# Performance work log

Hardware: AMD Instinct MI355X
Metric: run time of the kernel (lower is better)

Reference implementation:

```python
import jax, jax.numpy as jnp
import numpy as np

B = 4096
STATE_DIM = 64
OBS_DIM = 32
BASE_DEGREE = 8
TIME_STEPS = 96
EPS = 1e-7


def _degree(t):
    # get_degree: degree_params initialized to linspace(0,1,time_steps); used via .item() (static)
    p = float(t) / (TIME_STEPS - 1)
    scaled = 0.5 * (1.0 + np.sin(2.0 * np.pi * p))
    return BASE_DEGREE + int(2.0 * scaled)


def _cheby_fwd_and_jac(x, coeffs, degree):
    """ChebyKAN forward y[b,o] = sum_{i,d} coeffs[i,o,d] * cos(d*acos(clip(tanh(x[b,i]))))
    plus its analytic per-sample Jacobian J[b,o,i] (replaces the torch autograd loop)."""
    t_raw = jnp.tanh(x)                                   # [B, D]
    t_val = jnp.clip(t_raw, -1.0 + EPS, 1.0 - EPS)
    theta = jnp.arccos(t_val)                             # [B, D]
    dvals = jnp.arange(degree + 1, dtype=x.dtype)         # [deg+1]
    ang = theta[..., None] * dvals                        # [B, D, deg+1]
    cheb = jnp.cos(ang)
    ac = coeffs[..., : degree + 1]                        # [D, D, deg+1]
    y = jnp.einsum('bid,iod->bo', cheb, ac)               # [B, D]
    # d cheb / d x = d*sin(d*theta) * (1 - tanh(x)^2) * mask / sqrt(1 - t_val^2)
    mask = ((t_raw > -1.0 + EPS) & (t_raw < 1.0 - EPS)).astype(x.dtype)
    dtheta_dx = -(1.0 - t_raw * t_raw) * mask / jnp.sqrt(1.0 - t_val * t_val)  # [B, D]
    dcheb_dx = -dvals * jnp.sin(ang) * dtheta_dx[..., None]                    # [B, D, deg+1]
    jac = jnp.einsum('bid,iod->boi', dcheb_dx, ac)        # [B, D, D] = dY_o/dx_i
    return y, jac


def setup_inputs() -> dict:
    key = jax.random.key(0)
    ks = jax.random.split(key, 5)
    obs = jax.random.normal(ks[0], (B, OBS_DIM), jnp.float32)
    prev_state = jax.random.normal(ks[1], (B, STATE_DIM), jnp.float32)
    A = jax.random.normal(ks[2], (B, STATE_DIM, STATE_DIM), jnp.float32)
    prev_cov = A @ A.transpose(0, 2, 1) / STATE_DIM + jnp.eye(STATE_DIM, dtype=jnp.float32)  # SPD
    bound = 1.0 / np.sqrt(STATE_DIM * (BASE_DEGREE + 3))  # kaiming-uniform style
    coeffs = jax.random.uniform(ks[3], (STATE_DIM, STATE_DIM, BASE_DEGREE + 3), jnp.float32, -bound, bound)
    M = jax.random.normal(ks[4], (STATE_DIM, OBS_DIM), jnp.float32)
    q, _ = jnp.linalg.qr(M)                               # orthonormal columns
    obs_matrix = q.T.astype(jnp.float32)                  # [OBS_DIM, STATE_DIM], orthogonal rows
    log_Q_diag = jnp.zeros((STATE_DIM,), jnp.float32)
    log_R_diag = jnp.zeros((OBS_DIM,), jnp.float32)
    return dict(obs=obs, prev_state=prev_state, prev_cov=prev_cov, coeffs=coeffs,
                obs_matrix=obs_matrix, log_Q_diag=log_Q_diag, log_R_diag=log_R_diag, t=10)


def reference(obs, prev_state, prev_cov, coeffs, obs_matrix, log_Q_diag, log_R_diag, t):
    degree = _degree(t)
    state_pred, Fj = _cheby_fwd_and_jac(prev_state, coeffs, degree)   # [B,D], [B,D,D]
    q = jnp.exp(log_Q_diag)                                           # [D]
    r = jnp.exp(log_R_diag)                                           # [O]
    H = obs_matrix                                                    # [O, D]
    # cov_pred = F P F^T + Q
    cov_pred = jnp.einsum('bij,bjk,blk->bil', Fj, prev_cov, Fj) + jnp.diag(q)[None]
    obs_pred = state_pred @ H.T                                       # [B, O]
    residual = obs - obs_pred                                         # [B, O]
    # S = H Pp H^T + R
    S = jnp.einsum('ij,bjk,lk->bil', H, cov_pred, H) + jnp.diag(r)[None]
    S_inv = jnp.linalg.pinv(S)                                        # [B, O, O]
    PHt = jnp.einsum('bij,oj->bio', cov_pred, H)                      # [B, D, O]
    K = jnp.einsum('bio,bop->bip', PHt, S_inv)                        # [B, D, O]
    state_update = state_pred + jnp.einsum('bio,bo->bi', K, residual)
    I_KH = jnp.eye(STATE_DIM, dtype=cov_pred.dtype)[None] - jnp.einsum('bio,oj->bij', K, H)
    # Joseph form: (I-KH) Pp (I-KH)^T + K R K^T
    cov_update = (jnp.einsum('bij,bjk,blk->bil', I_KH, cov_pred, I_KH)
                  + jnp.einsum('bio,o,bjo->bij', K, r, K))
    cov_diag = jnp.diagonal(cov_update, axis1=1, axis2=2)
    return state_update, cov_update, cov_diag
```

## Files before the change

kernel.cpp:

```cpp
#include <hip/hip_runtime.h>
#include <math.h>


typedef float f4 __attribute__((ext_vector_type(4)));
typedef float f32x4 __attribute__((ext_vector_type(4)));
typedef short b16x8 __attribute__((ext_vector_type(8)));
typedef short b16x4 __attribute__((ext_vector_type(4)));
typedef unsigned int u32;
typedef unsigned int u32x4 __attribute__((ext_vector_type(4)));
typedef unsigned short u16;

#define EPSC 1e-7f
#define MFMA(a, b, c) __builtin_amdgcn_mfma_f32_16x16x32_bf16(a, b, c, 0, 0, 0)
static constexpr size_t CU_OFF = 4096 * 64;
static constexpr size_t CD_OFF = CU_OFF + 4096ull * 4096;

__device__ __forceinline__ void split2(float x, short &h, short &l) {
  u32 u = __float_as_uint(x);
  h = (short)(u >> 16);
  float rem = x - __uint_as_float(u & 0xffff0000u);
  l = (short)(__float_as_uint(rem) >> 16);
}
__device__ __forceinline__ u32 packsplit(float x) {
  u32 u = __float_as_uint(x) & 0xffff0000u;
  float rem = x - __uint_as_float(u);
  return u | (__float_as_uint(rem) >> 16);
}
__device__ __forceinline__ float unpackf(u32 v) {
  return __uint_as_float(v & 0xffff0000u) + __uint_as_float(v << 16);
}
union U8 { u32x4 u; b16x8 s; };
__device__ __forceinline__ void unpack8(u32x4 q0, u32x4 q1, b16x8 &hi,
                                        b16x8 &lo) {
  U8 H, L;
  H.u[0] = __builtin_amdgcn_perm(q0[1], q0[0], 0x07060302u);
  H.u[1] = __builtin_amdgcn_perm(q0[3], q0[2], 0x07060302u);
  H.u[2] = __builtin_amdgcn_perm(q1[1], q1[0], 0x07060302u);
  H.u[3] = __builtin_amdgcn_perm(q1[3], q1[2], 0x07060302u);
  L.u[0] = __builtin_amdgcn_perm(q0[1], q0[0], 0x05040100u);
  L.u[1] = __builtin_amdgcn_perm(q0[3], q0[2], 0x05040100u);
  L.u[2] = __builtin_amdgcn_perm(q1[1], q1[0], 0x05040100u);
  L.u[3] = __builtin_amdgcn_perm(q1[3], q1[2], 0x05040100u);
  hi = H.s;
  lo = L.s;
}
__device__ __forceinline__ void split8v(f4 a, f4 b, b16x8 &hi, b16x8 &lo) {
#pragma unroll
  for (int j = 0; j < 4; ++j) {
    short hh, ll;
    split2(a[j], hh, ll); hi[j] = hh; lo[j] = ll;
    split2(b[j], hh, ll); hi[4 + j] = hh; lo[4 + j] = ll;
  }
}

__global__ __launch_bounds__(256, 4) void kalman_fused(
    const float *__restrict__ obs, const float *__restrict__ prev_state,
    const float *__restrict__ prev_cov, const float *__restrict__ coeffs,
    const float *__restrict__ Hm, const float *__restrict__ logQ,
    const float *__restrict__ logR, const int *__restrict__ tptr,
    float *__restrict__ out) {
  __shared__ __align__(16) unsigned char pool[32768];
  u16 *sPh = (u16 *)(pool);
  u16 *sPl = (u16 *)(pool + 8192);
  u32 *sT = (u32 *)(pool);
  u32 *sPHt = (u32 *)(pool);
  u32 *sSpk = (u32 *)(pool + 8192);
  u32 *sK = (u32 *)(pool + 8192);
  u16 *sFh = (u16 *)(pool + 16384);
  u16 *sFl = (u16 *)(pool + 24576);
  u32 *sCov = (u32 *)(pool + 16384);
  float *sChT = (float *)(pool);
  float *sDcT = (float *)(pool + 3072);
  float *ypart = (float *)(pool + 6144);

  const int tid = (int)threadIdx.x;
  const int b = (int)blockIdx.x;
  const int w = tid >> 6;
  const int l = tid & 63;
  const int lr = l & 15;
  const int h = l >> 4;
  const int rowbase = (w == 0) ? 48 : 16 * (w - 1);

  f4 pr[4];
  {
    const float *Pg = prev_cov + (size_t)b * 4096;
#pragma unroll
    for (int e = 0; e < 4; ++e)
      pr[e] = *(const f4 *)(Pg + (rowbase + 4 * e + h) * 64 + lr * 4);
    if (tid < 64) {
      const int tval = tptr[0];
      const float ang = 6.28318530717958647f * ((float)tval / 95.0f);
      const int D = 9 + (int)(1.0f + sinf(ang));
      const float xx = prev_state[b * 64 + tid];
      const float tr_ = tanhf(xx);
      const float tv = fminf(fmaxf(tr_, -1.0f + EPSC), 1.0f - EPSC);
      const float sn = sqrtf(fmaxf(1.0f - tv * tv, 0.0f));
      const float mask = (tr_ > -1.0f + EPSC && tr_ < 1.0f - EPSC) ? 1.0f : 0.0f;
      const float dth = -(1.0f - tr_ * tr_) * mask / sn;
      float *ct = sChT + tid * 12;
      float *dt = sDcT + tid * 12;
      ct[0] = 1.f; ct[1] = tv; ct[11] = 0.f;
      dt[0] = 0.f; dt[1] = -dth * sn; dt[11] = 0.f;
      float cm2 = 1.f, cm1 = tv, sm2 = 0.f, sm1 = sn;
      const float tv2 = 2.f * tv;
#pragma unroll
      for (int d = 2; d <= 10; ++d) {
        const float cc = fmaf(tv2, cm1, -cm2);
        const float ss = fmaf(tv2, sm1, -sm2);
        ct[d] = (d < D) ? cc : 0.f;
        dt[d] = (d < D) ? (-dth * (float)d * ss) : 0.f;
        cm2 = cm1; cm1 = cc; sm2 = sm1; sm1 = ss;
      }
    }
  }
  __syncthreads();

  {
    const int o = tid & 63, g = tid >> 6;
    float yacc = 0.f;
    float fr[16];
#pragma unroll
    for (int ii = 0; ii < 16; ++ii) {
      const int i = g * 16 + ii;
      const float *cp = coeffs + (size_t)(i * 64 + o) * 11;
      f4 q0 = *(const f4 *)(cp);
      f4 q1 = *(const f4 *)(cp + 4);
      f4 q2 = *(const f4 *)(cp + 7);
      const float *ct = sChT + i * 12;
      const float *dt = sDcT + i * 12;
      f4 c0 = *(const f4 *)(ct), c1 = *(const f4 *)(ct + 4),
         c2 = *(const f4 *)(ct + 8);
      f4 e0 = *(const f4 *)(dt), e1 = *(const f4 *)(dt + 4),
         e2 = *(const f4 *)(dt + 8);
      float yac = q0[0];
      yac = fmaf(q0[1], c0[1], yac);
      yac = fmaf(q0[2], c0[2], yac);
      yac = fmaf(q0[3], c0[3], yac);
      yac = fmaf(q1[0], c1[0], yac);
      yac = fmaf(q1[1], c1[1], yac);
      yac = fmaf(q1[2], c1[2], yac);
      yac = fmaf(q1[3], c1[3], yac);
      yac = fmaf(q2[1], c2[0], yac);
      yac = fmaf(q2[2], c2[1], yac);
      yac = fmaf(q2[3], c2[2], yac);
      float fra = q0[1] * e0[1];
      fra = fmaf(q0[2], e0[2], fra);
      fra = fmaf(q0[3], e0[3], fra);
      fra = fmaf(q1[0], e1[0], fra);
      fra = fmaf(q1[1], e1[1], fra);
      fra = fmaf(q1[2], e1[2], fra);
      fra = fmaf(q1[3], e1[3], fra);
      fra = fmaf(q2[1], e2[0], fra);
      fra = fmaf(q2[2], e2[1], fra);
      fra = fmaf(q2[3], e2[2], fra);
      yacc += yac;
      fr[ii] = fra;
    }
    b16x8 fh0, fh1, fl0, fl1;
#pragma unroll
    for (int j = 0; j < 8; ++j) {
      short hh, ll;
      split2(fr[j], hh, ll); fh0[j] = hh; fl0[j] = ll;
      split2(fr[8 + j], hh, ll); fh1[j] = hh; fl1[j] = ll;
    }
    const int x = (o & 7) << 3;
    *(b16x8 *)(sFh + o * 64 + ((g * 16) ^ x)) = fh0;
    *(b16x8 *)(sFh + o * 64 + ((g * 16 + 8) ^ x)) = fh1;
    *(b16x8 *)(sFl + o * 64 + ((g * 16) ^ x)) = fl0;
    *(b16x8 *)(sFl + o * 64 + ((g * 16 + 8) ^ x)) = fl1;
    ypart[g * 64 + o] = yacc;
  }
  __syncthreads();

  float syl = 0.f, residreg = 0.f;
  if (w == 0)
    syl = ypart[l] + ypart[64 + l] + ypart[128 + l] + ypart[192 + l];
#pragma unroll
  for (int e = 0; e < 4; ++e) {
    const int row = rowbase + 4 * e + h;
    const int x = (row & 7) << 3;
    b16x4 h4, l4;
#pragma unroll
    for (int j = 0; j < 4; ++j) {
      short hh, ll;
      split2(pr[e][j], hh, ll);
      h4[j] = hh; l4[j] = ll;
    }
    *(b16x4 *)(sPh + row * 64 + ((lr * 4) ^ x)) = h4;
    *(b16x4 *)(sPl + row * 64 + ((lr * 4) ^ x)) = l4;
  }
  if (w == 0) {
    const int r = l & 31;
    float racc = obs[b * 32 + r];
    const float *Hr = Hm + r * 64;
#pragma unroll
    for (int c = 0; c < 64; c += 4) {
      f4 hv = *(const f4 *)(Hr + c);
#pragma unroll
      for (int j = 0; j < 4; ++j)
        racc = fmaf(-hv[j], __shfl(syl, c + j, 64), racc);
    }
    residreg = racc;
  }
  __syncthreads();

  f32x4 accT[4] = {{0.f, 0.f, 0.f, 0.f}, {0.f, 0.f, 0.f, 0.f},
                   {0.f, 0.f, 0.f, 0.f}, {0.f, 0.f, 0.f, 0.f}};
  {
    const int m = 16 * w + lr;
    const int xA = (m & 7) << 3;
#pragma unroll
    for (int kc = 0; kc < 2; ++kc) {
      const int k = kc * 32 + h * 8;
      b16x8 Ah = *(const b16x8 *)(sFh + m * 64 + (k ^ xA));
      b16x8 Al = *(const b16x8 *)(sFl + m * 64 + (k ^ xA));
#pragma unroll
      for (int t = 0; t < 4; ++t) {
        const int n = t * 16 + lr;
        const int xB = (n & 7) << 3;
        b16x8 Bh = *(const b16x8 *)(sPh + n * 64 + (k ^ xB));
        b16x8 Bl = *(const b16x8 *)(sPl + n * 64 + (k ^ xB));
        accT[t] = MFMA(Ah, Bh, accT[t]);
        accT[t] = MFMA(Al, Bh, accT[t]);
        accT[t] = MFMA(Ah, Bl, accT[t]);
      }
    }
  }
  __syncthreads();
  {
    const int r0 = 16 * w + h * 4;
#pragma unroll
    for (int t = 0; t < 4; ++t)
#pragma unroll
      for (int j = 0; j < 4; ++j) {
        const int rr = r0 + j, cc = t * 16 + lr;
        sT[rr * 64 + (cc ^ ((rr & 7) << 2))] = packsplit(accT[t][j]);
      }
  }

  f32x4 accC[4] = {{0.f, 0.f, 0.f, 0.f}, {0.f, 0.f, 0.f, 0.f},
                   {0.f, 0.f, 0.f, 0.f}, {0.f, 0.f, 0.f, 0.f}};
  {
    const int m = 16 * w + lr;
    const int xA = (m & 7) << 2;
    const u32 *Tb = sT + m * 64;
#pragma unroll
    for (int kc = 0; kc < 2; ++kc) {
      const int k = kc * 32 + h * 8;
      u32x4 q0 = *(const u32x4 *)(Tb + (k ^ xA));
      u32x4 q1 = *(const u32x4 *)(Tb + ((k + 4) ^ xA));
      b16x8 Ah, Al;
      unpack8(q0, q1, Ah, Al);
#pragma unroll
      for (int t = 0; t < 4; ++t) {
        const int n = t * 16 + lr;
        const int xB = (n & 7) << 3;
        b16x8 Bh = *(const b16x8 *)(sFh + n * 64 + (k ^ xB));
        b16x8 Bl = *(const b16x8 *)(sFl + n * 64 + (k ^ xB));
        accC[t] = MFMA(Ah, Bh, accC[t]);
        accC[t] = MFMA(Al, Bh, accC[t]);
        accC[t] = MFMA(Ah, Bl, accC[t]);
      }
    }
  }
  __syncthreads();
  {
    const int r0 = 16 * w + h * 4;
    f4 lq = *(const f4 *)(logQ + r0);
    float qv[4];
#pragma unroll
    for (int j = 0; j < 4; ++j) qv[j] = expf(lq[j]);
#pragma unroll
    for (int t = 0; t < 4; ++t)
#pragma unroll
      for (int j = 0; j < 4; ++j) {
        const int rr = r0 + j, cc = t * 16 + lr;
        float v = accC[t][j];
        if (rr == cc) v += qv[j];
        sCov[rr * 64 + (cc ^ ((rr & 7) << 2))] = packsplit(v);
      }
  }

  {
    f32x4 acc[2] = {{0.f, 0.f, 0.f, 0.f}, {0.f, 0.f, 0.f, 0.f}};
    const int m = 16 * w + lr;
    const int xA = (m & 7) << 2;
    const u32 *Cb = sCov + m * 64;
#pragma unroll
    for (int kc = 0; kc < 2; ++kc) {
      const int k = kc * 32 + h * 8;
      u32x4 q0 = *(const u32x4 *)(Cb + (k ^ xA));
      u32x4 q1 = *(const u32x4 *)(Cb + ((k + 4) ^ xA));
      b16x8 Ah, Al;
      unpack8(q0, q1, Ah, Al);
#pragma unroll
      for (int t = 0; t < 2; ++t) {
        const int n = t * 16 + lr;
        const float *Hr = Hm + n * 64 + k;
        f4 b0 = *(const f4 *)(Hr);
        f4 b1 = *(const f4 *)(Hr + 4);
        b16x8 Bh, Bl;
        split8v(b0, b1, Bh, Bl);
        acc[t] = MFMA(Ah, Bh, acc[t]);
        acc[t] = MFMA(Al, Bh, acc[t]);
        acc[t] = MFMA(Ah, Bl, acc[t]);
      }
    }
    const int r0 = 16 * w + h * 4;
#pragma unroll
    for (int t = 0; t < 2; ++t)
#pragma unroll
      for (int j = 0; j < 4; ++j) {
        const int rr = r0 + j, cc = t * 16 + lr;
        sPHt[rr * 32 + (cc ^ ((rr & 7) << 2))] = packsplit(acc[t][j]);
      }
  }
  __syncthreads();

  {
    const int tr = w >> 1, tc = w & 1;
    f32x4 acc = {0.f, 0.f, 0.f, 0.f};
    const int m = tr * 16 + lr;
    const int n = tc * 16 + lr;
#pragma unroll
    for (int kc = 0; kc < 2; ++kc) {
      const int k = kc * 32 + h * 8;
      const float *Hr = Hm + m * 64 + k;
      f4 a0 = *(const f4 *)(Hr);
      f4 a1 = *(const f4 *)(Hr + 4);
      b16x8 Ah, Al;
      split8v(a0, a1, Ah, Al);
      u32x4 q0, q1;
#pragma unroll
      for (int j = 0; j < 4; ++j)
        q0[j] = sPHt[(k + j) * 32 + (n ^ (j << 2))];
#pragma unroll
      for (int j = 0; j < 4; ++j)
        q1[j] = sPHt[(k + 4 + j) * 32 + (n ^ ((4 + j) << 2))];
      b16x8 Bh, Bl;
      unpack8(q0, q1, Bh, Bl);
      acc = MFMA(Ah, Bh, acc);
      acc = MFMA(Al, Bh, acc);
      acc = MFMA(Ah, Bl, acc);
    }
    const int r0s = tr * 16 + h * 4;
    f4 lrv = *(const f4 *)(logR + r0s);
#pragma unroll
    for (int j = 0; j < 4; ++j) {
      const int rr = r0s + j, cc = tc * 16 + lr;
      float v = acc[j];
      if (rr == cc) v += expf(lrv[j]);
      sSpk[rr * 32 + (cc ^ ((rr & 7) << 2))] = packsplit(v);
    }
  }
  __syncthreads();

  if (w == 0) {
    const int mr = l >> 1, half = l & 1;
    const int xm = (mr & 7) << 2;
    float s0[16];
#pragma unroll
    for (int qi = 0; qi < 4; ++qi) {
      u32x4 qv = *(const u32x4 *)(sSpk + mr * 32 + ((half * 16 + qi * 4) ^ xm));
#pragma unroll
      for (int j = 0; j < 4; ++j) s0[qi * 4 + j] = unpackf(qv[j]);
    }
#pragma unroll
    for (int p = 0; p < 32; ++p) {
      const int ph = p >> 4, pi = p & 15;
      float prow[16];
#pragma unroll
      for (int j = 0; j < 16; ++j) prow[j] = __shfl(s0[j], 2 * p + half, 64);
      const float dpp = __shfl(s0[pi], 2 * p + ph, 64);
      const float d = 1.0f / dpp;
      const float fv = __shfl(s0[pi], (l & 62) + ph, 64);
      if (mr == p) {
#pragma unroll
        for (int j = 0; j < 16; ++j) s0[j] = prow[j] * d;
        if (half == ph) s0[pi] = d;
      } else {
        const float fd = fv * d;
#pragma unroll
        for (int j = 0; j < 16; ++j) s0[j] = fmaf(-fd, prow[j], s0[j]);
        if (half == ph) s0[pi] = -fd;
      }
    }
#pragma unroll
    for (int qi = 0; qi < 4; ++qi) {
      u32x4 ov;
#pragma unroll
      for (int j = 0; j < 4; ++j) ov[j] = packsplit(s0[qi * 4 + j]);
      *(u32x4 *)(sSpk + mr * 32 + ((half * 16 + qi * 4) ^ xm)) = ov;
    }
  }
  __syncthreads();

  f32x4 accK[2] = {{0.f, 0.f, 0.f, 0.f}, {0.f, 0.f, 0.f, 0.f}};
  {
    const int m = 16 * w + lr;
    const int xA = (m & 7) << 2;
    const int k = h * 8;
    u32x4 q0 = *(const u32x4 *)(sPHt + m * 32 + (k ^ xA));
    u32x4 q1 = *(const u32x4 *)(sPHt + m * 32 + ((k + 4) ^ xA));
    b16x8 Ah, Al;
    unpack8(q0, q1, Ah, Al);
#pragma unroll
    for (int t = 0; t < 2; ++t) {
      const int n = t * 16 + lr;
      const int xB = (n & 7) << 2;
      u32x4 b0 = *(const u32x4 *)(sSpk + n * 32 + (k ^ xB));
      u32x4 b1 = *(const u32x4 *)(sSpk + n * 32 + ((k + 4) ^ xB));
      b16x8 Bh, Bl;
      unpack8(b0, b1, Bh, Bl);
      accK[t] = MFMA(Ah, Bh, accK[t]);
      accK[t] = MFMA(Al, Bh, accK[t]);
      accK[t] = MFMA(Ah, Bl, accK[t]);
    }
  }
  __syncthreads();
  {
    const int r0 = 16 * w + h * 4;
#pragma unroll
    for (int t = 0; t < 2; ++t)
#pragma unroll
      for (int j = 0; j < 4; ++j) {
        const int rr = r0 + j, cc = t * 16 + lr;
        sK[rr * 32 + (cc ^ ((rr & 7) << 2))] = packsplit(accK[t][j]);
      }
  }
  __syncthreads();

  if (tid < 64) {
    float su = syl;
    const int x = (l & 7) << 2;
    const u32 *Kb = sK + l * 32;
#pragma unroll
    for (int c0 = 0; c0 < 32; c0 += 4) {
      u32x4 q = *(const u32x4 *)(Kb + (c0 ^ x));
#pragma unroll
      for (int j = 0; j < 4; ++j)
        su = fmaf(unpackf(q[j]), __shfl(residreg, c0 + j, 64), su);
    }
    out[b * 64 + l] = su;
  }
  {
    const int m = 16 * w + lr;
    const int xA = (m & 7) << 2;
    const int k = h * 8;
    u32x4 q0 = *(const u32x4 *)(sK + m * 32 + (k ^ xA));
    u32x4 q1 = *(const u32x4 *)(sK + m * 32 + ((k + 4) ^ xA));
#pragma unroll
    for (int j = 0; j < 4; ++j) {
      q0[j] ^= 0x80008000u;
      q1[j] ^= 0x80008000u;
    }
    b16x8 Ah, Al;
    unpack8(q0, q1, Ah, Al);
    const int r0 = 16 * w + h * 4;
    float *outc = out + CU_OFF + (size_t)b * 4096;
#pragma unroll
    for (int t = 0; t < 4; ++t) {
      const int n = t * 16 + lr;
      const int xB = (n & 7) << 2;
      u32x4 p0 = *(const u32x4 *)(sPHt + n * 32 + (k ^ xB));
      u32x4 p1 = *(const u32x4 *)(sPHt + n * 32 + ((k + 4) ^ xB));
      b16x8 Bh, Bl;
      unpack8(p0, p1, Bh, Bl);
      f32x4 acc;
#pragma unroll
      for (int j = 0; j < 4; ++j) {
        const int rr = r0 + j;
        acc[j] = unpackf(sCov[rr * 64 + (n ^ ((rr & 7) << 2))]);
      }
      acc = MFMA(Ah, Bh, acc);
      acc = MFMA(Al, Bh, acc);
      acc = MFMA(Ah, Bl, acc);
#pragma unroll
      for (int j = 0; j < 4; ++j) {
        const int rr = r0 + j;
        outc[rr * 64 + n] = acc[j];
        if (rr == n) out[CD_OFF + b * 64 + rr] = acc[j];
      }
    }
  }
}

extern "C" void kernel_launch(void *const *d_in, const int *in_sizes, int n_in,
                              void *d_out, int out_size, void *d_ws,
                              size_t ws_size, hipStream_t stream) {
  const float *obs = (const float *)d_in[0];
  const float *prev_state = (const float *)d_in[1];
  const float *prev_cov = (const float *)d_in[2];
  const float *coeffs = (const float *)d_in[3];
  const float *Hm = (const float *)d_in[4];
  const float *logQ = (const float *)d_in[5];
  const float *logR = (const float *)d_in[6];
  const int *tptr = (const int *)d_in[7];
  (void)in_sizes; (void)n_in; (void)out_size; (void)d_ws; (void)ws_size;
  kalman_fused<<<dim3(4096), dim3(256), 0, stream>>>(
      obs, prev_state, prev_cov, coeffs, Hm, logQ, logR, tptr, (float *)d_out);
}
```

Baseline: 142.9 us.

## Recompute Chebyshev terms per thread and split prev_cov into LDS immediately

Each thread now evaluates the Chebyshev and derivative recurrences inline from per-input tanh values and dtheta stored in LDS, instead of building shared tables of cheb and dcheb values. prev_cov is loaded in a contiguous coalesced pattern and split into bf16 hi/lo LDS tiles straight away, so the P tile no longer waits in registers across barriers. The y reduction and residual are reordered to reuse wave 0's own partial sum. This trades redundant ALU work (the recurrence is recomputed 64 times per input) for fewer LDS reads and writes and lower register pressure.

New measurement: 266.7 us. +86.6%, slower.

```diff
diff --git a/kernel.cpp b/kernel.cpp
--- a/kernel.cpp
+++ b/kernel.cpp
@@ -69,9 +69,7 @@
   u16 *sFh = (u16 *)(pool + 16384);
   u16 *sFl = (u16 *)(pool + 24576);
   u32 *sCov = (u32 *)(pool + 16384);
-  float *sChT = (float *)(pool);
-  float *sDcT = (float *)(pool + 3072);
-  float *ypart = (float *)(pool + 6144);
+  float *R2f = (float *)(pool + 16384);
 
   const int tid = (int)threadIdx.x;
   const int b = (int)blockIdx.x;
@@ -79,83 +77,98 @@
   const int l = tid & 63;
   const int lr = l & 15;
   const int h = l >> 4;
-  const int rowbase = (w == 0) ? 48 : 16 * (w - 1);
-
-  f4 pr[4];
+
+  const int tval = tptr[0];
+  const float ang = 6.28318530717958647f * ((float)tval / 95.0f);
+  const int D = 9 + (int)(1.0f + sinf(ang));
+
   {
     const float *Pg = prev_cov + (size_t)b * 4096;
 #pragma unroll
-    for (int e = 0; e < 4; ++e)
-      pr[e] = *(const f4 *)(Pg + (rowbase + 4 * e + h) * 64 + lr * 4);
+    for (int e = 0; e < 4; ++e) {
+      const int idx = tid + 256 * e;
+      f4 v = *(const f4 *)(Pg + 4 * idx);
+      const int r = idx >> 4, c = (idx & 15) * 4;
+      const int x = (r & 7) << 3;
+      b16x4 h4, l4;
+#pragma unroll
+      for (int j = 0; j < 4; ++j) {
+        short hh, ll;
+        split2(v[j], hh, ll);
+        h4[j] = hh; l4[j] = ll;
+      }
+      *(b16x4 *)(sPh + r * 64 + (c ^ x)) = h4;
+      *(b16x4 *)(sPl + r * 64 + (c ^ x)) = l4;
+    }
     if (tid < 64) {
-      const int tval = tptr[0];
-      const float ang = 6.28318530717958647f * ((float)tval / 95.0f);
-      const int D = 9 + (int)(1.0f + sinf(ang));
       const float xx = prev_state[b * 64 + tid];
       const float tr_ = tanhf(xx);
       const float tv = fminf(fmaxf(tr_, -1.0f + EPSC), 1.0f - EPSC);
       const float sn = sqrtf(fmaxf(1.0f - tv * tv, 0.0f));
       const float mask = (tr_ > -1.0f + EPSC && tr_ < 1.0f - EPSC) ? 1.0f : 0.0f;
-      const float dth = -(1.0f - tr_ * tr_) * mask / sn;
-      float *ct = sChT + tid * 12;
-      float *dt = sDcT + tid * 12;
-      ct[0] = 1.f; ct[1] = tv; ct[11] = 0.f;
-      dt[0] = 0.f; dt[1] = -dth * sn; dt[11] = 0.f;
-      float cm2 = 1.f, cm1 = tv, sm2 = 0.f, sm1 = sn;
-      const float tv2 = 2.f * tv;
-#pragma unroll
-      for (int d = 2; d <= 10; ++d) {
-        const float cc = fmaf(tv2, cm1, -cm2);
-        const float ss = fmaf(tv2, sm1, -sm2);
-        ct[d] = (d < D) ? cc : 0.f;
-        dt[d] = (d < D) ? (-dth * (float)d * ss) : 0.f;
-        cm2 = cm1; cm1 = cc; sm2 = sm1; sm1 = ss;
-      }
-    }
-  }
-  __syncthreads();
-
+      R2f[tid] = tv;
+      R2f[64 + tid] = -(1.0f - tr_ * tr_) * mask / sn;
+    }
+  }
+  __syncthreads();
+
+  float yacc = 0.f;
+  float fr[16];
   {
     const int o = tid & 63, g = tid >> 6;
-    float yacc = 0.f;
-    float fr[16];
 #pragma unroll
     for (int ii = 0; ii < 16; ++ii) {
       const int i = g * 16 + ii;
+      const float tv = R2f[i], dth = R2f[64 + i];
+      const float sn = sqrtf(fmaxf(1.0f - tv * tv, 0.0f));
       const float *cp = coeffs + (size_t)(i * 64 + o) * 11;
       f4 q0 = *(const f4 *)(cp);
       f4 q1 = *(const f4 *)(cp + 4);
       f4 q2 = *(const f4 *)(cp + 7);
-      const float *ct = sChT + i * 12;
-      const float *dt = sDcT + i * 12;
-      f4 c0 = *(const f4 *)(ct), c1 = *(const f4 *)(ct + 4),
-         c2 = *(const f4 *)(ct + 8);
-      f4 e0 = *(const f4 *)(dt), e1 = *(const f4 *)(dt + 4),
-         e2 = *(const f4 *)(dt + 8);
-      float yac = q0[0];
-      yac = fmaf(q0[1], c0[1], yac);
-      yac = fmaf(q0[2], c0[2], yac);
-      yac = fmaf(q0[3], c0[3], yac);
-      yac = fmaf(q1[0], c1[0], yac);
-      yac = fmaf(q1[1], c1[1], yac);
-      yac = fmaf(q1[2], c1[2], yac);
-      yac = fmaf(q1[3], c1[3], yac);
-      yac = fmaf(q2[1], c2[0], yac);
-      yac = fmaf(q2[2], c2[1], yac);
-      yac = fmaf(q2[3], c2[2], yac);
-      float fra = q0[1] * e0[1];
-      fra = fmaf(q0[2], e0[2], fra);
-      fra = fmaf(q0[3], e0[3], fra);
-      fra = fmaf(q1[0], e1[0], fra);
-      fra = fmaf(q1[1], e1[1], fra);
-      fra = fmaf(q1[2], e1[2], fra);
-      fra = fmaf(q1[3], e1[3], fra);
-      fra = fmaf(q2[1], e2[0], fra);
-      fra = fmaf(q2[2], e2[1], fra);
-      fra = fmaf(q2[3], e2[2], fra);
+      float cy[11];
+#pragma unroll
+      for (int j = 0; j < 4; ++j) { cy[j] = q0[j]; cy[4 + j] = q1[j]; }
+      cy[8] = q2[1]; cy[9] = q2[2]; cy[10] = q2[3];
+      if (D < 10) cy[9] = 0.f;
+      if (D < 11) cy[10] = 0.f;
+      float yac = fmaf(cy[1], tv, cy[0]);
+      float wac = cy[1] * sn;
+      float cm2 = 1.f, cm1 = tv, sm2 = 0.f, sm1 = sn;
+      const float tv2 = 2.f * tv;
+#pragma unroll
+      for (int d = 2; d <= 10; ++d) {
+        const float cc = fmaf(tv2, cm1, -cm2);
+        const float ss = fmaf(tv2, sm1, -sm2);
+        yac = fmaf(cy[d], cc, yac);
+        wac = fmaf(cy[d] * (float)d, ss, wac);
+        cm2 = cm1; cm1 = cc; sm2 = sm1; sm1 = ss;
+      }
       yacc += yac;
-      fr[ii] = fra;
-    }
+      fr[ii] = -dth * wac;
+    }
+    if (w > 0) R2f[128 + (w - 1) * 64 + o] = yacc;
+  }
+  __syncthreads();
+
+  float syl = 0.f, residreg = 0.f;
+  if (w == 0) {
+    syl = yacc + R2f[128 + l] + R2f[192 + l] + R2f[256 + l];
+    const int r = l & 31;
+    float racc = obs[b * 32 + r];
+    const float *Hr = Hm + r * 64;
+#pragma unroll
+    for (int c = 0; c < 64; c += 4) {
+      f4 hv = *(const f4 *)(Hr + c);
+#pragma unroll
+      for (int j = 0; j < 4; ++j)
+        racc = fmaf(-hv[j], __shfl(syl, c + j, 64), racc);
+    }
+    residreg = racc;
+  }
+  __syncthreads();
+
+  {
+    const int o = tid & 63, g = tid >> 6;
     b16x8 fh0, fh1, fl0, fl1;
 #pragma unroll
     for (int j = 0; j < 8; ++j) {
@@ -168,39 +181,6 @@
     *(b16x8 *)(sFh + o * 64 + ((g * 16 + 8) ^ x)) = fh1;
     *(b16x8 *)(sFl + o * 64 + ((g * 16) ^ x)) = fl0;
     *(b16x8 *)(sFl + o * 64 + ((g * 16 + 8) ^ x)) = fl1;
-    ypart[g * 64 + o] = yacc;
-  }
-  __syncthreads();
-
-  float syl = 0.f, residreg = 0.f;
-  if (w == 0)
-    syl = ypart[l] + ypart[64 + l] + ypart[128 + l] + ypart[192 + l];
-#pragma unroll
-  for (int e = 0; e < 4; ++e) {
-    const int row = rowbase + 4 * e + h;
-    const int x = (row & 7) << 3;
-    b16x4 h4, l4;
-#pragma unroll
-    for (int j = 0; j < 4; ++j) {
-      short hh, ll;
-      split2(pr[e][j], hh, ll);
-      h4[j] = hh; l4[j] = ll;
-    }
-    *(b16x4 *)(sPh + row * 64 + ((lr * 4) ^ x)) = h4;
-    *(b16x4 *)(sPl + row * 64 + ((lr * 4) ^ x)) = l4;
-  }
-  if (w == 0) {
-    const int r = l & 31;
-    float racc = obs[b * 32 + r];
-    const float *Hr = Hm + r * 64;
-#pragma unroll
-    for (int c = 0; c < 64; c += 4) {
-      f4 hv = *(const f4 *)(Hr + c);
-#pragma unroll
-      for (int j = 0; j < 4; ++j)
-        racc = fmaf(-hv[j], __shfl(syl, c + j, 64), racc);
-    }
-    residreg = racc;
   }
   __syncthreads();
 
```
